# Kernel optimization log

Measured on AMD Instinct MI355X. Metric: run time of the kernel, lower is better.

## Reference

```python
import jax, jax.numpy as jnp
import numpy as np

N_NODES = 50000
N_EDGES = 400000


def setup_inputs() -> dict:
    key = jax.random.key(0)
    ks = jax.random.split(key, 8)
    d_in, d_hid, d_out = 512, 512, 256
    feats = jax.random.normal(ks[0], (N_NODES, d_in), dtype=jnp.float32)
    src = jax.random.randint(ks[1], (N_EDGES,), 0, N_NODES, dtype=jnp.int32)
    dst = jax.random.randint(ks[2], (N_EDGES,), 0, N_NODES, dtype=jnp.int32)
    # Glorot-ish scaled weights so activations stay O(1)
    W0 = jax.random.normal(ks[3], (d_in, d_hid), dtype=jnp.float32) / np.sqrt(d_in)
    b0 = jnp.zeros((d_hid,), jnp.float32)
    W1 = jax.random.normal(ks[4], (d_hid, d_hid), dtype=jnp.float32) / np.sqrt(d_hid)
    b1 = jnp.zeros((d_hid,), jnp.float32)
    W2 = jax.random.normal(ks[5], (d_hid, d_out), dtype=jnp.float32) / np.sqrt(d_hid)
    b2 = jnp.zeros((d_out,), jnp.float32)
    return {"feats": feats, "src": src, "dst": dst,
            "W0": W0, "b0": b0, "W1": W1, "b1": b1, "W2": W2, "b2": b2}


def _sage_conv_gcn(h, src, dst, W, b, deg):
    # DGL SAGEConv aggregator_type='gcn':
    # h_neigh[v] = (sum_{u->v} h[u] + h[v]) / (in_deg(v) + 1); out = h_neigh @ W + b
    agg = jax.ops.segment_sum(h[src], dst, num_segments=h.shape[0])  # [N, d]
    h_neigh = (agg + h) / (deg[:, None] + 1.0)
    return h_neigh @ W + b


def reference(feats, src, dst, W0, b0, W1, b1, W2, b2):
    N = feats.shape[0]
    deg = jax.ops.segment_sum(jnp.ones((src.shape[0],), feats.dtype), dst,
                              num_segments=N)  # in-degree per node
    h = jax.nn.relu(_sage_conv_gcn(feats, src, dst, W0, b0, deg))  # dropout p=0, norm none
    h = jax.nn.relu(_sage_conv_gcn(h, src, dst, W1, b1, deg))
    h = _sage_conv_gcn(h, src, dst, W2, b2, deg)  # final layer: no activation
    return h
```

## Files before the change

### kernel.cpp

```cpp
#include <hip/hip_runtime.h>
#include <stdint.h>

#define N_NODES 50000
#define N_EDGES 400000
#define MPAD    50048
#define SCAN_B  49
#define G_GEMM  1564
#define H_BLKS  1563

typedef __bf16 bf16x8 __attribute__((ext_vector_type(8)));
typedef float  f32x4  __attribute__((ext_vector_type(4)));
typedef unsigned short ushort_t;
typedef unsigned int   uint_t;

__device__ __forceinline__ ushort_t f2b(float f){
    uint_t x = __float_as_uint(f);
    x += 0x7FFFu + ((x >> 16) & 1u);
    return (ushort_t)(x >> 16);
}
__device__ __forceinline__ float b2f(ushort_t h){
    return __uint_as_float(((uint_t)h) << 16);
}

__device__ __forceinline__ int xcd_swz(int orig, int nwg){
    int q = nwg >> 3, r = nwg & 7;
    int xcd = orig & 7, idx = orig >> 3;
    int base = (xcd < r) ? xcd * (q + 1) : r * (q + 1) + (xcd - r) * q;
    return base + idx;
}

__global__ __launch_bounds__(256) void pre_kernel(
        const float* __restrict__ W0, const float* __restrict__ W1,
        const float* __restrict__ W2, ushort_t* __restrict__ W0t,
        ushort_t* __restrict__ W1t, ushort_t* __restrict__ W2t,
        int* __restrict__ deg, int* __restrict__ cursor){
    int b = blockIdx.x;
    if (b >= 640){
        int i = (b - 640) * 256 + threadIdx.x;
        if (i < N_NODES){ deg[i] = 0; cursor[i] = 0; }
        return;
    }
    __shared__ float t[32][33];
    const float* W; ushort_t* Wt; int K, N, bx, by;
    if (b < 256){            W = W0; Wt = W0t; K = 512; N = 512;
                             bx = (b & 15) * 32; by = (b >> 4) * 32; }
    else if (b < 512){ b -= 256; W = W1; Wt = W1t; K = 512; N = 512;
                             bx = (b & 15) * 32; by = (b >> 4) * 32; }
    else {             b -= 512; W = W2; Wt = W2t; K = 512; N = 256;
                             bx = (b & 7) * 32;  by = (b >> 3) * 32; }
    const int x = threadIdx.x & 31, y = threadIdx.x >> 5;
    #pragma unroll
    for (int j = 0; j < 32; j += 8)
        t[y + j][x] = W[(size_t)(by + y + j) * N + bx + x];
    __syncthreads();
    #pragma unroll
    for (int j = 0; j < 32; j += 8)
        Wt[(size_t)(bx + y + j) * K + by + x] = f2b(t[x][y + j]);
}

__global__ __launch_bounds__(1024) void blk_scan_kernel(
        const int* __restrict__ deg, int* __restrict__ offs,
        int* __restrict__ bsum, int n){
    __shared__ int buf[1024];
    const int t = threadIdx.x, b = blockIdx.x;
    const int i = b * 1024 + t;
    int v = (i < n) ? deg[i] : 0;
    buf[t] = v; __syncthreads();
    for (int off = 1; off < 1024; off <<= 1){
        int x = (t >= off) ? buf[t - off] : 0;
        __syncthreads();
        buf[t] += x;
        __syncthreads();
    }
    if (i < n) offs[i] = buf[t] - v;
    if (t == 1023) bsum[b] = buf[1023];
}

__global__ __launch_bounds__(1024) void add_off2_kernel(
        int* __restrict__ offs, const int* __restrict__ bsum, int n){
    __shared__ int boff;
    if (threadIdx.x < 64){
        int t = threadIdx.x;
        int own = (t < SCAN_B) ? bsum[t] : 0;
        int v = own;
        #pragma unroll
        for (int off = 1; off < 64; off <<= 1){
            int x = __shfl_up(v, off, 64);
            if (t >= off) v += x;
        }
        if (t == blockIdx.x) boff = v - own;
    }
    __syncthreads();
    int i = blockIdx.x * 1024 + threadIdx.x;
    if (i < n) offs[i] += boff;
    if (i == 0) offs[n] = N_EDGES;
}

__global__ void fill_kernel(const int* __restrict__ src, const int* __restrict__ dst,
                            const int* __restrict__ offs, int* __restrict__ cursor,
                            int* __restrict__ nbr, int E){
    int i = blockIdx.x * blockDim.x + threadIdx.x;
    if (i < E){
        int d = dst[i];
        int p = atomicAdd(&cursor[d], 1);
        nbr[offs[d] + p] = src[i];
    }
}

__device__ __forceinline__ void load16(const void* g, void* l){
    __builtin_amdgcn_global_load_lds((const __attribute__((address_space(1))) void*)g,
                                     (__attribute__((address_space(3))) void*)l, 16, 0, 0);
}

__global__ __launch_bounds__(256, 4) void gemm128_bt(const ushort_t* __restrict__ A,
                                                     const ushort_t* __restrict__ Bt,
                                                     ushort_t* __restrict__ C,
                                                     int NBN, int N, int K){
    __shared__ ushort_t As[128 * 64];
    __shared__ ushort_t Bs[128 * 64];
    const int tid  = threadIdx.x, lane = tid & 63, wave = tid >> 6;
    const int wg = xcd_swz(blockIdx.x, gridDim.x);
    const int bm = wg / NBN, bn = wg - bm * NBN;
    const int fr = lane & 15;
    const int wm = (wave >> 1) * 64, wn = (wave & 1) * 64;
    f32x4 acc[4][4] = {};

    for (int kt = 0; kt < K; kt += 64){
        __syncthreads();
        #pragma unroll
        for (int i = 0; i < 4; i++){
            int s = tid + i * 256;
            int row = s >> 3, p = s & 7, c = p ^ (row & 7);
            load16(A + (size_t)(bm * 128 + row) * K + kt + c * 8,
                   (char*)As + s * 16);
        }
        #pragma unroll
        for (int i = 0; i < 4; i++){
            int s = tid + i * 256;
            int row = s >> 3, p = s & 7, c = p ^ (row & 7);
            load16(Bt + (size_t)(bn * 128 + row) * K + kt + c * 8,
                   (char*)Bs + s * 16);
        }
        __syncthreads();
        #pragma unroll
        for (int ks = 0; ks < 2; ks++){
            const int c = (lane >> 4) + ks * 4;
            const int cx = c ^ (fr & 7);
            bf16x8 af[4], bf[4];
            #pragma unroll
            for (int t = 0; t < 4; t++)
                af[t] = *(const bf16x8*)(const void*)(As + (wm + t * 16 + fr) * 64 + cx * 8);
            #pragma unroll
            for (int t = 0; t < 4; t++)
                bf[t] = *(const bf16x8*)(const void*)(Bs + (wn + t * 16 + fr) * 64 + cx * 8);
            #pragma unroll
            for (int tm = 0; tm < 4; tm++)
                #pragma unroll
                for (int tn = 0; tn < 4; tn++)
                    acc[tm][tn] = __builtin_amdgcn_mfma_f32_16x16x32_bf16(
                                      af[tm], bf[tn], acc[tm][tn], 0, 0, 0);
        }
    }
    const int r0 = (lane >> 4) * 4, c0 = lane & 15;
    #pragma unroll
    for (int tm = 0; tm < 4; tm++){
        #pragma unroll
        for (int tn = 0; tn < 4; tn++){
            int rbase = bm * 128 + wm + tm * 16 + r0;
            int cidx  = bn * 128 + wn + tn * 16 + c0;
            #pragma unroll
            for (int reg = 0; reg < 4; reg++)
                C[(size_t)(rbase + reg) * N + cidx] = f2b(acc[tm][tn][reg]);
        }
    }
}

__global__ __launch_bounds__(256, 4) void gemm128_a32h(const float* __restrict__ A,
                                                       const ushort_t* __restrict__ Bt,
                                                       ushort_t* __restrict__ C,
                                                       const int* __restrict__ dst,
                                                       int* __restrict__ deg,
                                                       int K){
    __shared__ ushort_t As[128 * 64];
    __shared__ ushort_t Bs[128 * 64];
    if (blockIdx.x >= G_GEMM){
        int i = (blockIdx.x - G_GEMM) * 256 + threadIdx.x;
        if (i < N_EDGES) atomicAdd(&deg[dst[i]], 1);
        return;
    }
    const int tid  = threadIdx.x, lane = tid & 63, wave = tid >> 6;
    const int wg = xcd_swz(blockIdx.x, G_GEMM);
    const int bm = wg >> 2, bn = wg & 3;
    const int fr = lane & 15;
    const int wm = (wave >> 1) * 64, wn = (wave & 1) * 64;
    f32x4 acc[4][4] = {};

    for (int kt = 0; kt < K; kt += 64){
        __syncthreads();
        float4 x[4], y[4];
        #pragma unroll
        for (int i = 0; i < 4; i++){
            int s = tid + i * 256;
            int row = s >> 3, p = s & 7, c = p ^ (row & 7);
            int grow = bm * 128 + row;
            if (grow < N_NODES){
                const float* pp = A + (size_t)grow * K + kt + c * 8;
                x[i] = *(const float4*)(const void*)pp;
                y[i] = *(const float4*)(const void*)(pp + 4);
            } else {
                x[i] = make_float4(0.f, 0.f, 0.f, 0.f);
                y[i] = make_float4(0.f, 0.f, 0.f, 0.f);
            }
        }
        #pragma unroll
        for (int i = 0; i < 4; i++){
            int s = tid + i * 256;
            int row = s >> 3, p = s & 7, c = p ^ (row & 7);
            load16(Bt + (size_t)(bn * 128 + row) * K + kt + c * 8,
                   (char*)Bs + s * 16);
        }
        #pragma unroll
        for (int i = 0; i < 4; i++){
            int s = tid + i * 256;
            uint4 o;
            o.x = (uint_t)f2b(x[i].x) | ((uint_t)f2b(x[i].y) << 16);
            o.y = (uint_t)f2b(x[i].z) | ((uint_t)f2b(x[i].w) << 16);
            o.z = (uint_t)f2b(y[i].x) | ((uint_t)f2b(y[i].y) << 16);
            o.w = (uint_t)f2b(y[i].z) | ((uint_t)f2b(y[i].w) << 16);
            *(uint4*)(void*)((char*)As + s * 16) = o;
        }
        __syncthreads();
        #pragma unroll
        for (int ks = 0; ks < 2; ks++){
            const int c = (lane >> 4) + ks * 4;
            const int cx = c ^ (fr & 7);
            bf16x8 af[4], bf[4];
            #pragma unroll
            for (int t = 0; t < 4; t++)
                af[t] = *(const bf16x8*)(const void*)(As + (wm + t * 16 + fr) * 64 + cx * 8);
            #pragma unroll
            for (int t = 0; t < 4; t++)
                bf[t] = *(const bf16x8*)(const void*)(Bs + (wn + t * 16 + fr) * 64 + cx * 8);
            #pragma unroll
            for (int tm = 0; tm < 4; tm++)
                #pragma unroll
                for (int tn = 0; tn < 4; tn++)
                    acc[tm][tn] = __builtin_amdgcn_mfma_f32_16x16x32_bf16(
                                      af[tm], bf[tn], acc[tm][tn], 0, 0, 0);
        }
    }
    const int r0 = (lane >> 4) * 4, c0 = lane & 15;
    #pragma unroll
    for (int tm = 0; tm < 4; tm++){
        #pragma unroll
        for (int tn = 0; tn < 4; tn++){
            int rbase = bm * 128 + wm + tm * 16 + r0;
            int cidx  = bn * 128 + wn + tn * 16 + c0;
            #pragma unroll
            for (int reg = 0; reg < 4; reg++)
                C[(size_t)(rbase + reg) * 512 + cidx] = f2b(acc[tm][tn][reg]);
        }
    }
}

__device__ __forceinline__ void acc8(float* a, uint4 y){
    a[0] += b2f((ushort_t)(y.x & 0xffff)); a[1] += b2f((ushort_t)(y.x >> 16));
    a[2] += b2f((ushort_t)(y.y & 0xffff)); a[3] += b2f((ushort_t)(y.y >> 16));
    a[4] += b2f((ushort_t)(y.z & 0xffff)); a[5] += b2f((ushort_t)(y.z >> 16));
    a[6] += b2f((ushort_t)(y.w & 0xffff)); a[7] += b2f((ushort_t)(y.w >> 16));
}
__device__ __forceinline__ void acc4(float* a, uint2 y){
    a[0] += b2f((ushort_t)(y.x & 0xffff)); a[1] += b2f((ushort_t)(y.x >> 16));
    a[2] += b2f((ushort_t)(y.y & 0xffff)); a[3] += b2f((ushort_t)(y.y >> 16));
}

__global__ __launch_bounds__(256) void agg_relu_kernel(
        const ushort_t* __restrict__ Y, const int* __restrict__ offs,
        const int* __restrict__ nbr, const float* __restrict__ bias,
        ushort_t* __restrict__ H){
    const int lane = threadIdx.x & 63, wave = threadIdx.x >> 6;
    const int v0 = blockIdx.x * 8 + wave * 2, v1 = v0 + 1;
    const int off = lane * 8;
    float a0[8], a1[8];
    {   uint4 y = *(const uint4*)(const void*)(Y + (size_t)v0 * 512 + off);
        a0[0] = b2f((ushort_t)(y.x & 0xffff)); a0[1] = b2f((ushort_t)(y.x >> 16));
        a0[2] = b2f((ushort_t)(y.y & 0xffff)); a0[3] = b2f((ushort_t)(y.y >> 16));
        a0[4] = b2f((ushort_t)(y.z & 0xffff)); a0[5] = b2f((ushort_t)(y.z >> 16));
        a0[6] = b2f((ushort_t)(y.w & 0xffff)); a0[7] = b2f((ushort_t)(y.w >> 16)); }
    {   uint4 y = *(const uint4*)(const void*)(Y + (size_t)v1 * 512 + off);
        a1[0] = b2f((ushort_t)(y.x & 0xffff)); a1[1] = b2f((ushort_t)(y.x >> 16));
        a1[2] = b2f((ushort_t)(y.y & 0xffff)); a1[3] = b2f((ushort_t)(y.y >> 16));
        a1[4] = b2f((ushort_t)(y.z & 0xffff)); a1[5] = b2f((ushort_t)(y.z >> 16));
        a1[6] = b2f((ushort_t)(y.w & 0xffff)); a1[7] = b2f((ushort_t)(y.w >> 16)); }
    const int beg0 = offs[v0], end0 = offs[v0 + 1];
    const int beg1 = offs[v1], end1 = offs[v1 + 1];
    int i0 = beg0, i1 = beg1;
    while (i0 + 4 <= end0 && i1 + 4 <= end1){
        uint4 yy0[4], yy1[4];
        #pragma unroll
        for (int j = 0; j < 4; j++){
            int u = nbr[i0 + j];
            yy0[j] = *(const uint4*)(const void*)(Y + (size_t)u * 512 + off);
        }
        #pragma unroll
        for (int j = 0; j < 4; j++){
            int u = nbr[i1 + j];
            yy1[j] = *(const uint4*)(const void*)(Y + (size_t)u * 512 + off);
        }
        #pragma unroll
        for (int j = 0; j < 4; j++) acc8(a0, yy0[j]);
        #pragma unroll
        for (int j = 0; j < 4; j++) acc8(a1, yy1[j]);
        i0 += 4; i1 += 4;
    }
    for (; i0 + 4 <= end0; i0 += 4){
        uint4 yy[4];
        #pragma unroll
        for (int j = 0; j < 4; j++){
            int u = nbr[i0 + j];
            yy[j] = *(const uint4*)(const void*)(Y + (size_t)u * 512 + off);
        }
        #pragma unroll
        for (int j = 0; j < 4; j++) acc8(a0, yy[j]);
    }
    for (; i0 < end0; i0++){
        int u = nbr[i0];
        uint4 y = *(const uint4*)(const void*)(Y + (size_t)u * 512 + off);
        acc8(a0, y);
    }
    for (; i1 + 4 <= end1; i1 += 4){
        uint4 yy[4];
        #pragma unroll
        for (int j = 0; j < 4; j++){
            int u = nbr[i1 + j];
            yy[j] = *(const uint4*)(const void*)(Y + (size_t)u * 512 + off);
        }
        #pragma unroll
        for (int j = 0; j < 4; j++) acc8(a1, yy[j]);
    }
    for (; i1 < end1; i1++){
        int u = nbr[i1];
        uint4 y = *(const uint4*)(const void*)(Y + (size_t)u * 512 + off);
        acc8(a1, y);
    }
    float4 bb0 = ((const float4*)bias)[lane * 2];
    float4 bb1 = ((const float4*)bias)[lane * 2 + 1];
    {
        const float inv = 1.0f / (float)(end0 - beg0 + 1);
        float r[8];
        r[0] = a0[0]*inv + bb0.x; r[1] = a0[1]*inv + bb0.y;
        r[2] = a0[2]*inv + bb0.z; r[3] = a0[3]*inv + bb0.w;
        r[4] = a0[4]*inv + bb1.x; r[5] = a0[5]*inv + bb1.y;
        r[6] = a0[6]*inv + bb1.z; r[7] = a0[7]*inv + bb1.w;
        #pragma unroll
        for (int j = 0; j < 8; j++) r[j] = r[j] > 0.f ? r[j] : 0.f;
        uint4 o;
        o.x = (uint_t)f2b(r[0]) | ((uint_t)f2b(r[1]) << 16);
        o.y = (uint_t)f2b(r[2]) | ((uint_t)f2b(r[3]) << 16);
        o.z = (uint_t)f2b(r[4]) | ((uint_t)f2b(r[5]) << 16);
        o.w = (uint_t)f2b(r[6]) | ((uint_t)f2b(r[7]) << 16);
        *(uint4*)(void*)(H + (size_t)v0 * 512 + off) = o;
    }
    {
        const float inv = 1.0f / (float)(end1 - beg1 + 1);
        float r[8];
        r[0] = a1[0]*inv + bb0.x; r[1] = a1[1]*inv + bb0.y;
        r[2] = a1[2]*inv + bb0.z; r[3] = a1[3]*inv + bb0.w;
        r[4] = a1[4]*inv + bb1.x; r[5] = a1[5]*inv + bb1.y;
        r[6] = a1[6]*inv + bb1.z; r[7] = a1[7]*inv + bb1.w;
        #pragma unroll
        for (int j = 0; j < 8; j++) r[j] = r[j] > 0.f ? r[j] : 0.f;
        uint4 o;
        o.x = (uint_t)f2b(r[0]) | ((uint_t)f2b(r[1]) << 16);
        o.y = (uint_t)f2b(r[2]) | ((uint_t)f2b(r[3]) << 16);
        o.z = (uint_t)f2b(r[4]) | ((uint_t)f2b(r[5]) << 16);
        o.w = (uint_t)f2b(r[6]) | ((uint_t)f2b(r[7]) << 16);
        *(uint4*)(void*)(H + (size_t)v1 * 512 + off) = o;
    }
}

__global__ __launch_bounds__(256) void agg_out_kernel(
        const ushort_t* __restrict__ Y, const int* __restrict__ offs,
        const int* __restrict__ nbr, const float* __restrict__ bias,
        float* __restrict__ out){
    const int lane = threadIdx.x & 63, wave = threadIdx.x >> 6;
    const int v = blockIdx.x * 4 + wave;
    const int off = lane * 4;
    float a[4];
    {   uint2 y = *(const uint2*)(const void*)(Y + (size_t)v * 256 + off);
        a[0] = b2f((ushort_t)(y.x & 0xffff)); a[1] = b2f((ushort_t)(y.x >> 16));
        a[2] = b2f((ushort_t)(y.y & 0xffff)); a[3] = b2f((ushort_t)(y.y >> 16)); }
    const int beg = offs[v], end = offs[v + 1];
    int i = beg;
    for (; i + 8 <= end; i += 8){
        uint2 yy[8];
        #pragma unroll
        for (int j = 0; j < 8; j++){
            int u = nbr[i + j];
            yy[j] = *(const uint2*)(const void*)(Y + (size_t)u * 256 + off);
        }
        #pragma unroll
        for (int j = 0; j < 8; j++) acc4(a, yy[j]);
    }
    for (; i + 4 <= end; i += 4){
        uint2 yy[4];
        #pragma unroll
        for (int j = 0; j < 4; j++){
            int u = nbr[i + j];
            yy[j] = *(const uint2*)(const void*)(Y + (size_t)u * 256 + off);
        }
        #pragma unroll
        for (int j = 0; j < 4; j++) acc4(a, yy[j]);
    }
    for (; i < end; i++){
        int u = nbr[i];
        uint2 y = *(const uint2*)(const void*)(Y + (size_t)u * 256 + off);
        acc4(a, y);
    }
    const float inv = 1.0f / (float)(end - beg + 1);
    float4 bb = ((const float4*)bias)[lane];
    float4 r;
    r.x = a[0]*inv + bb.x; r.y = a[1]*inv + bb.y;
    r.z = a[2]*inv + bb.z; r.w = a[3]*inv + bb.w;
    ((float4*)out)[v * 64 + lane] = r;
}

extern "C" void kernel_launch(void* const* d_in, const int* in_sizes, int n_in,
                              void* d_out, int out_size, void* d_ws, size_t ws_size,
                              hipStream_t stream) {
    const float* feats = (const float*)d_in[0];
    const int*   src   = (const int*)  d_in[1];
    const int*   dst   = (const int*)  d_in[2];
    const float* W0    = (const float*)d_in[3];
    const float* b0    = (const float*)d_in[4];
    const float* W1    = (const float*)d_in[5];
    const float* b1    = (const float*)d_in[6];
    const float* W2    = (const float*)d_in[7];
    const float* b2    = (const float*)d_in[8];
    float* out = (float*)d_out;

    char* w = (char*)d_ws;
    ushort_t* Abuf = (ushort_t*)w;  w += (size_t)MPAD * 512 * 2;
    ushort_t* Ybuf = (ushort_t*)w;  w += (size_t)MPAD * 512 * 2;
    ushort_t* W0t  = (ushort_t*)w;  w += 512 * 512 * 2;
    ushort_t* W1t  = (ushort_t*)w;  w += 512 * 512 * 2;
    ushort_t* W2t  = (ushort_t*)w;  w += 256 * 512 * 2;
    int* deg    = (int*)w;          w += 50048 * 4;
    int* offs   = (int*)w;          w += 50056 * 4;
    int* cursor = (int*)w;          w += 50048 * 4;
    int* nbr    = (int*)w;          w += (size_t)N_EDGES * 4;
    int* bsum   = (int*)w;          w += 64 * 4;

    pre_kernel<<<836, 256, 0, stream>>>(W0, W1, W2, W0t, W1t, W2t, deg, cursor);
    gemm128_a32h<<<G_GEMM + H_BLKS, 256, 0, stream>>>(feats, W0t, Ybuf, dst, deg, 512);
    blk_scan_kernel<<<SCAN_B, 1024, 0, stream>>>(deg, offs, bsum, N_NODES);
    add_off2_kernel<<<SCAN_B, 1024, 0, stream>>>(offs, bsum, N_NODES);
    fill_kernel<<<H_BLKS, 256, 0, stream>>>(src, dst, offs, cursor, nbr, N_EDGES);
    agg_relu_kernel<<<N_NODES / 8, 256, 0, stream>>>(Ybuf, offs, nbr, b0, Abuf);
    gemm128_bt<<<(MPAD / 128) * 4, 256, 0, stream>>>(Abuf, W1t, Ybuf, 4, 512, 512);
    agg_relu_kernel<<<N_NODES / 8, 256, 0, stream>>>(Ybuf, offs, nbr, b1, Abuf);
    gemm128_bt<<<(MPAD / 128) * 2, 256, 0, stream>>>(Abuf, W2t, Ybuf, 2, 256, 512);
    agg_out_kernel<<<N_NODES / 4, 256, 0, stream>>>(Ybuf, offs, nbr, b2, out);
}
```

Before: 466.2 us.

## Fuse two-pass scan into one kernel and prefetch next K-tile in GEMM

The two scan launches are merged into one kernel. Each block recomputes all 49 chunk sums itself and takes its own prefix offset, which removes a kernel launch and the bsum round trip but adds redundant reads of deg. The bf16 GEMM now loads both k-substeps of fragments from LDS into registers, syncs, and starts the global-to-LDS load of the next K tile before running the MFMAs, so memory traffic overlaps compute. This doubles the fragment registers held per thread, which may reduce occupancy.

```diff
diff --git a/kernel.cpp b/kernel.cpp
--- a/kernel.cpp
+++ b/kernel.cpp
@@ -58,11 +58,37 @@
         Wt[(size_t)(bx + y + j) * K + by + x] = f2b(t[x][y + j]);
 }
 
-__global__ __launch_bounds__(1024) void blk_scan_kernel(
-        const int* __restrict__ deg, int* __restrict__ offs,
-        int* __restrict__ bsum, int n){
+__global__ __launch_bounds__(1024) void scan_fused(const int* __restrict__ deg,
+                                                   int* __restrict__ offs, int n){
     __shared__ int buf[1024];
+    __shared__ int csum[64];
+    __shared__ int cpre[64];
     const int t = threadIdx.x, b = blockIdx.x;
+    const int lane = t & 63, wv = t >> 6;
+    for (int c = wv; c < SCAN_B; c += 16){
+        int s = 0;
+        #pragma unroll
+        for (int j = 0; j < 16; j++){
+            int i = c * 1024 + j * 64 + lane;
+            s += (i < n) ? deg[i] : 0;
+        }
+        #pragma unroll
+        for (int off = 32; off; off >>= 1) s += __shfl_down(s, off, 64);
+        if (lane == 0) csum[c] = s;
+    }
+    __syncthreads();
+    if (wv == 0){
+        int own = (lane < SCAN_B) ? csum[lane] : 0;
+        int v = own;
+        #pragma unroll
+        for (int off = 1; off < 64; off <<= 1){
+            int x = __shfl_up(v, off, 64);
+            if (lane >= off) v += x;
+        }
+        if (lane < SCAN_B) cpre[lane] = v - own;
+    }
+    __syncthreads();
+    const int boff = cpre[b];
     const int i = b * 1024 + t;
     int v = (i < n) ? deg[i] : 0;
     buf[t] = v; __syncthreads();
@@ -72,27 +98,7 @@
         buf[t] += x;
         __syncthreads();
     }
-    if (i < n) offs[i] = buf[t] - v;
-    if (t == 1023) bsum[b] = buf[1023];
-}
-
-__global__ __launch_bounds__(1024) void add_off2_kernel(
-        int* __restrict__ offs, const int* __restrict__ bsum, int n){
-    __shared__ int boff;
-    if (threadIdx.x < 64){
-        int t = threadIdx.x;
-        int own = (t < SCAN_B) ? bsum[t] : 0;
-        int v = own;
-        #pragma unroll
-        for (int off = 1; off < 64; off <<= 1){
-            int x = __shfl_up(v, off, 64);
-            if (t >= off) v += x;
-        }
-        if (t == blockIdx.x) boff = v - own;
-    }
-    __syncthreads();
-    int i = blockIdx.x * 1024 + threadIdx.x;
-    if (i < n) offs[i] += boff;
+    if (i < n) offs[i] = buf[t] - v + boff;
     if (i == 0) offs[n] = N_EDGES;
 }
 
@@ -125,41 +131,43 @@
     const int wm = (wave >> 1) * 64, wn = (wave & 1) * 64;
     f32x4 acc[4][4] = {};
 
-    for (int kt = 0; kt < K; kt += 64){
-        __syncthreads();
+    const ushort_t* Ab = A  + (size_t)(bm * 128) * K;
+    const ushort_t* Bb = Bt + (size_t)(bn * 128) * K;
+
+    auto stage = [&](int kt){
         #pragma unroll
         for (int i = 0; i < 4; i++){
             int s = tid + i * 256;
             int row = s >> 3, p = s & 7, c = p ^ (row & 7);
-            load16(A + (size_t)(bm * 128 + row) * K + kt + c * 8,
-                   (char*)As + s * 16);
-        }
-        #pragma unroll
-        for (int i = 0; i < 4; i++){
-            int s = tid + i * 256;
-            int row = s >> 3, p = s & 7, c = p ^ (row & 7);
-            load16(Bt + (size_t)(bn * 128 + row) * K + kt + c * 8,
-                   (char*)Bs + s * 16);
-        }
-        __syncthreads();
+            load16(Ab + (size_t)row * K + kt + c * 8, (char*)As + s * 16);
+            load16(Bb + (size_t)row * K + kt + c * 8, (char*)Bs + s * 16);
+        }
+    };
+
+    stage(0);
+    const int NT = K >> 6;
+    for (int t = 0; t < NT; ++t){
+        __syncthreads();
+        bf16x8 af[2][4], bf[2][4];
         #pragma unroll
         for (int ks = 0; ks < 2; ks++){
-            const int c = (lane >> 4) + ks * 4;
-            const int cx = c ^ (fr & 7);
-            bf16x8 af[4], bf[4];
-            #pragma unroll
-            for (int t = 0; t < 4; t++)
-                af[t] = *(const bf16x8*)(const void*)(As + (wm + t * 16 + fr) * 64 + cx * 8);
-            #pragma unroll
-            for (int t = 0; t < 4; t++)
-                bf[t] = *(const bf16x8*)(const void*)(Bs + (wn + t * 16 + fr) * 64 + cx * 8);
+            const int cx = ((lane >> 4) + ks * 4) ^ (fr & 7);
+            #pragma unroll
+            for (int q = 0; q < 4; q++){
+                af[ks][q] = *(const bf16x8*)(const void*)(As + (wm + q * 16 + fr) * 64 + cx * 8);
+                bf[ks][q] = *(const bf16x8*)(const void*)(Bs + (wn + q * 16 + fr) * 64 + cx * 8);
+            }
+        }
+        __syncthreads();
+        if (t + 1 < NT) stage((t + 1) << 6);
+        #pragma unroll
+        for (int ks = 0; ks < 2; ks++)
             #pragma unroll
             for (int tm = 0; tm < 4; tm++)
                 #pragma unroll
                 for (int tn = 0; tn < 4; tn++)
                     acc[tm][tn] = __builtin_amdgcn_mfma_f32_16x16x32_bf16(
-                                      af[tm], bf[tn], acc[tm][tn], 0, 0, 0);
-        }
+                                      af[ks][tm], bf[ks][tn], acc[tm][tn], 0, 0, 0);
     }
     const int r0 = (lane >> 4) * 4, c0 = lane & 15;
     #pragma unroll
@@ -449,12 +457,10 @@
     int* offs   = (int*)w;          w += 50056 * 4;
     int* cursor = (int*)w;          w += 50048 * 4;
     int* nbr    = (int*)w;          w += (size_t)N_EDGES * 4;
-    int* bsum   = (int*)w;          w += 64 * 4;
 
     pre_kernel<<<836, 256, 0, stream>>>(W0, W1, W2, W0t, W1t, W2t, deg, cursor);
     gemm128_a32h<<<G_GEMM + H_BLKS, 256, 0, stream>>>(feats, W0t, Ybuf, dst, deg, 512);
-    blk_scan_kernel<<<SCAN_B, 1024, 0, stream>>>(deg, offs, bsum, N_NODES);
-    add_off2_kernel<<<SCAN_B, 1024, 0, stream>>>(offs, bsum, N_NODES);
+    scan_fused<<<SCAN_B, 1024, 0, stream>>>(deg, offs, N_NODES);
     fill_kernel<<<H_BLKS, 256, 0, stream>>>(src, dst, offs, cursor, nbr, N_EDGES);
     agg_relu_kernel<<<N_NODES / 8, 256, 0, stream>>>(Ybuf, offs, nbr, b0, Abuf);
     gemm128_bt<<<(MPAD / 128) * 4, 256, 0, stream>>>(Abuf, W1t, Ybuf, 4, 512, 512);
```

Result: slower. 556.7 us (+19.4%).
